# Kernel tuning notes

Hardware: AMD Instinct MI355X
Metric: run time of the kernel (lower is better)

The kernel has to match this reference:

```python
import jax, jax.numpy as jnp
import numpy as np

DROPOUT_P = 0.1  # original source passed p=1 (degenerate, zeros output); 0.1 used for a meaningful baseline


def setup_inputs() -> dict:
    key0 = jax.random.key(0)
    ks = jax.random.split(key0, 11)
    B, H, L, D, DQK, DV = 2, 8, 2048, 1024, 64, 64
    return {
        "query": jax.random.normal(ks[0], (B, H, L, D), jnp.float32),
        "key":   jax.random.normal(ks[1], (B, H, L, D), jnp.float32),
        "value": jax.random.normal(ks[2], (B, H, L, D), jnp.float32),
        "Wq": jax.random.normal(ks[3], (D, DQK), jnp.float32) * (D ** -0.5),
        "bq": jax.random.normal(ks[4], (DQK,), jnp.float32) * 0.02,
        "Wk": jax.random.normal(ks[5], (D, DQK), jnp.float32) * (D ** -0.5),
        "bk": jax.random.normal(ks[6], (DQK,), jnp.float32) * 0.02,
        "Wv": jax.random.normal(ks[7], (D, DV), jnp.float32) * (D ** -0.5),
        "bv": jax.random.normal(ks[8], (DV,), jnp.float32) * 0.02,
        "Wo": jax.random.normal(ks[9], (DV, D), jnp.float32) * (DV ** -0.5),
        "bo": jax.random.normal(ks[10], (D,), jnp.float32) * 0.02,
    }


def reference(query, key, value, Wq, bq, Wk, bk, Wv, bv, Wo, bo):
    # Per-head linear projections on 4D inputs (B,H,L,d_model)
    q = query @ Wq + bq            # (B,H,Lq,dqk)
    k = key @ Wk + bk              # (B,H,Lk,dqk)
    v = value @ Wv + bv            # (B,H,Lk,dv)
    # Quirky scale from source: q.size(2)*q.size(3)/key.size(2) * key.size(-1)**-0.5
    dk = (q.shape[2] * q.shape[3] / key.shape[2]) * (key.shape[-1] ** -0.5)
    scores = jnp.einsum('bhqd,bhkd->bhqk', q, k) * jnp.float32(dk)
    attn = jax.nn.softmax(scores, axis=-1)
    # Deterministic dropout with fixed key (inverted-scale, matching F.dropout)
    keep = jax.random.bernoulli(jax.random.key(42), 1.0 - DROPOUT_P, attn.shape)
    attn = jnp.where(keep, attn / (1.0 - DROPOUT_P), jnp.float32(0.0))
    out = jnp.einsum('bhqk,bhkd->bhqd', attn, v)  # (B,H,Lq,dv)
    return out @ Wo + bo                           # (B,H,Lq,d_model)
```

## Files before the change

### kernel.cpp

```cpp
#include <hip/hip_runtime.h>
#include <stdint.h>

typedef _Float16 f16;
typedef __attribute__((ext_vector_type(8))) _Float16 f16x8;
typedef __attribute__((ext_vector_type(4))) float f32x4;

__device__ __forceinline__ uint32_t rotl1(uint32_t x, uint32_t n){
  return __builtin_amdgcn_alignbit(x, x, 32u - n);
}
__device__ __forceinline__ uint32_t tf_bits(uint32_t i){
  const uint32_t ks1 = 42u, ks2 = 0x1BD11BDAu ^ 42u;
  uint32_t x0 = 0u, x1 = i + 42u;
#define R4(a,b,c,d) \
  x0 += x1; x1 = rotl1(x1,a); x1 ^= x0; \
  x0 += x1; x1 = rotl1(x1,b); x1 ^= x0; \
  x0 += x1; x1 = rotl1(x1,c); x1 ^= x0; \
  x0 += x1; x1 = rotl1(x1,d); x1 ^= x0;
  R4(13,15,26,6)  x0 += ks1; x1 += ks2 + 1u;
  R4(17,29,16,24) x0 += ks2; x1 += 2u;
  R4(13,15,26,6)               x1 += ks1 + 3u;
  R4(17,29,16,24) x0 += ks1; x1 += ks2 + 4u;
  R4(13,15,26,6)  x0 += ks2; x1 += 5u;
#undef R4
  return x0 ^ x1;
}

template<int PACKED>
__global__ __launch_bounds__(256) void proj_kernel(
    const float* __restrict__ query, const float* __restrict__ keyp, const float* __restrict__ value,
    const float* __restrict__ Wq, const float* __restrict__ bq,
    const float* __restrict__ Wk, const float* __restrict__ bk,
    const float* __restrict__ Wv, const float* __restrict__ bv,
    const float* __restrict__ Wo,
    f16* __restrict__ qp, f16* __restrict__ kp, f16* __restrict__ vpT,
    f16* __restrict__ WoT)
{
  __shared__ __align__(16) f16 Alds[64][40];
  __shared__ __align__(16) f16 Wlds[64][40];
  const int bid = blockIdx.x;
  const int tid = threadIdx.x;
  const int lane = tid & 63, wave = tid >> 6;
  const int llo = lane & 15, lhi = lane >> 4;

  int p;
  if (PACKED == 0){
    if (bid < 256){
      int t = bid*256 + tid;
      int n = t & 1023, k = t >> 10;
      WoT[(long)n*64 + k] = (f16)Wo[(long)k*1024 + n];
      return;
    }
    p = bid - 256;
  } else {
    p = 768 + bid;
  }

  const int which = p >> 9;
  const long m0 = (long)(p & 511) * 64;
  const float* A    = which==0 ? query : (which==1 ? keyp : value);
  const float* W    = which==0 ? Wq    : (which==1 ? Wk   : Wv);
  const float* bias = which==0 ? bq    : (which==1 ? bk   : bv);

  f32x4 acc[4];
  #pragma unroll
  for (int n=0;n<4;n++){
    float bb = bias[16*n + llo];
    acc[n][0]=bb; acc[n][1]=bb; acc[n][2]=bb; acc[n][3]=bb;
  }

  const int ar = tid >> 2;
  const int ac = (tid & 3) * 8;
  const int wcol = tid & 63;
  const int wk = (tid >> 6) * 8;

  for (int k0 = 0; k0 < 1024; k0 += 32){
    {
      const float* asrc = A + (m0 + ar)*1024 + k0 + ac;
      float4 v0 = *(const float4*)asrc;
      float4 v1 = *(const float4*)(asrc + 4);
      if (PACKED == 0){
        f16* ad = &Alds[ar][ac];
        ad[0]=(f16)v0.x; ad[1]=(f16)v0.y; ad[2]=(f16)v0.z; ad[3]=(f16)v0.w;
        ad[4]=(f16)v1.x; ad[5]=(f16)v1.y; ad[6]=(f16)v1.z; ad[7]=(f16)v1.w;
      } else {
        union { f16 h[8]; f16x8 v; } aw;
        aw.h[0]=(f16)v0.x; aw.h[1]=(f16)v0.y; aw.h[2]=(f16)v0.z; aw.h[3]=(f16)v0.w;
        aw.h[4]=(f16)v1.x; aw.h[5]=(f16)v1.y; aw.h[6]=(f16)v1.z; aw.h[7]=(f16)v1.w;
        *(f16x8*)&Alds[ar][ac] = aw.v;
      }
      f16 wt[8];
      #pragma unroll
      for (int j=0;j<8;j++) wt[j] = (f16)W[(long)(k0+wk+j)*64 + wcol];
      *(f16x8*)&Wlds[wcol][wk] = *(f16x8*)wt;
    }
    __syncthreads();
    f16x8 af = *(const f16x8*)&Alds[wave*16 + llo][lhi*8];
    #pragma unroll
    for (int n=0;n<4;n++){
      f16x8 bf = *(const f16x8*)&Wlds[16*n + llo][lhi*8];
      acc[n] = __builtin_amdgcn_mfma_f32_16x16x32_f16(af, bf, acc[n], 0,0,0);
    }
    __syncthreads();
  }

  if (which < 2){
    const float scale = (which==0) ? 2.0f : 1.0f;
    f16* dst = (which==0) ? qp : kp;
    #pragma unroll
    for (int n=0;n<4;n++)
      #pragma unroll
      for (int j=0;j<4;j++){
        long row = m0 + wave*16 + lhi*4 + j;
        dst[row*64 + 16*n + llo] = (f16)(acc[n][j]*scale);
      }
  } else {
    long row0 = m0 + wave*16 + lhi*4;
    long bh = row0 >> 11;
    long lr = row0 & 2047;
    #pragma unroll
    for (int n=0;n<4;n++){
      union { f16 h[4]; ushort4 u; } pk;
      #pragma unroll
      for (int j=0;j<4;j++) pk.h[j] = (f16)acc[n][j];
      *(ushort4*)&vpT[(bh*64 + 16*n + llo)*2048 + lr] = pk.u;
    }
  }
}

__global__ __launch_bounds__(256) void flash_kernel(
    const f16* __restrict__ qp, const f16* __restrict__ kp, const f16* __restrict__ vpT,
    float* __restrict__ Opart, float* __restrict__ Mp, float* __restrict__ Lp)
{
  __shared__ __align__(16) f16 Klds[64][72];
  __shared__ __align__(16) f16 Vlds[64][72];
  __shared__ __align__(16) f16 Plds[4][16][72];
  __shared__ unsigned short Idl[4][1024];
  const int tid = threadIdx.x;
  const int lane = tid & 63, wave = tid >> 6;
  const int llo = lane & 15, lhi = lane >> 4;
  const int bh = blockIdx.y;
  const int q0 = blockIdx.x * 64;
  const int kvh = blockIdx.z;

  const f16* qbase = qp + ((long)bh*2048 + q0 + wave*16 + llo)*64 + lhi*8;
  f16x8 qf0 = *(const f16x8*)qbase;
  f16x8 qf1 = *(const f16x8*)(qbase + 32);

  f32x4 O[4];
  float mrun[4], lrun[4];
  #pragma unroll
  for (int n=0;n<4;n++){ O[n][0]=0.f;O[n][1]=0.f;O[n][2]=0.f;O[n][3]=0.f; }
  #pragma unroll
  for (int j=0;j<4;j++){ mrun[j] = -__builtin_inff(); lrun[j]=0.f; }

  const int sr = tid >> 2;
  const int sc = (tid & 3) * 16;
  const f16* kbh = kp + (long)bh*2048*64;
  const f16* vbh = vpT + (long)bh*64*2048;
  uint32_t base_w = (uint32_t)((bh*2048 + q0 + wave*16)*2048) + (uint32_t)(kvh*1024);

  const int kvlo = kvh*1024, kvhi = kvlo + 1024;
  for (int kv0 = kvlo; kv0 < kvhi; kv0 += 64, base_w += 64u){
    {
      const f16* src = kbh + (long)(kv0 + sr)*64 + sc;
      f16x8 t0 = *(const f16x8*)src;
      f16x8 t1 = *(const f16x8*)(src+8);
      *(f16x8*)&Klds[sr][sc]   = t0;
      *(f16x8*)&Klds[sr][sc+8] = t1;
      const f16* vsrc = vbh + (long)sr*2048 + kv0 + sc;
      f16x8 u0 = *(const f16x8*)vsrc;
      f16x8 u1 = *(const f16x8*)(vsrc+8);
      *(f16x8*)&Vlds[sr][sc]   = u0;
      *(f16x8*)&Vlds[sr][sc+8] = u1;
    }
    __syncthreads();

    f32x4 s[4];
    #pragma unroll
    for (int n=0;n<4;n++){ s[n][0]=0.f;s[n][1]=0.f;s[n][2]=0.f;s[n][3]=0.f; }
    #pragma unroll
    for (int n=0;n<4;n++){
      f16x8 kf0 = *(const f16x8*)&Klds[16*n+llo][lhi*8];
      s[n] = __builtin_amdgcn_mfma_f32_16x16x32_f16(qf0, kf0, s[n], 0,0,0);
      f16x8 kf1 = *(const f16x8*)&Klds[16*n+llo][32+lhi*8];
      s[n] = __builtin_amdgcn_mfma_f32_16x16x32_f16(qf1, kf1, s[n], 0,0,0);
    }
    float pmax[4];
    #pragma unroll
    for (int j=0;j<4;j++)
      pmax[j] = fmaxf(fmaxf(s[0][j],s[1][j]), fmaxf(s[2][j],s[3][j]));
    #pragma unroll
    for (int off=1; off<16; off<<=1){
      #pragma unroll
      for (int j=0;j<4;j++) pmax[j] = fmaxf(pmax[j], __shfl_xor(pmax[j], off));
    }
    float esc[4];
    #pragma unroll
    for (int j=0;j<4;j++){
      float mnew = fmaxf(mrun[j], pmax[j]);
      esc[j] = __expf(mrun[j] - mnew);
      mrun[j] = mnew;
    }
    float p[4][4]; float lsum[4] = {0.f,0.f,0.f,0.f};
    #pragma unroll
    for (int n=0;n<4;n++)
      #pragma unroll
      for (int j=0;j<4;j++){
        p[n][j] = __expf(s[n][j] - mrun[j]);
        lsum[j] += p[n][j];
      }
    #pragma unroll
    for (int off=1; off<16; off<<=1){
      #pragma unroll
      for (int j=0;j<4;j++) lsum[j] += __shfl_xor(lsum[j], off);
    }
    #pragma unroll
    for (int j=0;j<4;j++) lrun[j] = lrun[j]*esc[j] + lsum[j];
    #pragma unroll
    for (int n=0;n<4;n++)
      #pragma unroll
      for (int j=0;j<4;j++) O[n][j] *= esc[j];

    uint32_t cnt = 0;
    #pragma unroll
    for (int j=0;j<4;j++){
      #pragma unroll
      for (int n=0;n<4;n++){
        float pm = p[n][j]*(1.0f/0.9f);
        bool surv = pm > 0x1.0p-25f;
        Plds[wave][lhi*4+j][16*n+llo] = (f16)pm;
        unsigned long long mk = __ballot(surv);
        if (mk){
          uint32_t pre = __builtin_amdgcn_mbcnt_hi((uint32_t)(mk>>32),
                         __builtin_amdgcn_mbcnt_lo((uint32_t)mk, 0u));
          if (surv)
            Idl[wave][cnt + pre] = (unsigned short)((j<<8)|(n<<6)|lane);
          cnt += (uint32_t)__builtin_popcountll(mk);
        }
      }
    }
    for (uint32_t pb = 0; pb < cnt; pb += 64){
      uint32_t idx = pb + (uint32_t)lane;
      if (idx < cnt){
        uint32_t id = (uint32_t)Idl[wave][idx];
        uint32_t jj = (id>>8)&3u, nn = (id>>6)&3u, ln = id & 63u;
        uint32_t i = base_w + (ln>>4)*8192u + jj*2048u + nn*16u + (ln&15u);
        uint32_t bits = tf_bits(i);
        if (bits >= 0xE6666600u)
          Plds[wave][(ln>>4)*4+jj][16*nn+(ln&15u)] = (f16)0;
      }
    }

    f16x8 pa0 = *(const f16x8*)&Plds[wave][llo][lhi*8];
    f16x8 pa1 = *(const f16x8*)&Plds[wave][llo][32+lhi*8];
    #pragma unroll
    for (int n=0;n<4;n++){
      f16x8 vf0 = *(const f16x8*)&Vlds[16*n+llo][lhi*8];
      O[n] = __builtin_amdgcn_mfma_f32_16x16x32_f16(pa0, vf0, O[n], 0,0,0);
      f16x8 vf1 = *(const f16x8*)&Vlds[16*n+llo][32+lhi*8];
      O[n] = __builtin_amdgcn_mfma_f32_16x16x32_f16(pa1, vf1, O[n], 0,0,0);
    }
    __syncthreads();
  }

  const long pr = ((long)kvh*16 + bh)*2048 + q0 + wave*16 + lhi*4;
  #pragma unroll
  for (int n=0;n<4;n++)
    #pragma unroll
    for (int j=0;j<4;j++)
      Opart[(pr + j)*64 + 16*n + llo] = O[n][j];
  if (llo == 0){
    const long mr = (long)kvh*32768 + bh*2048 + q0 + wave*16 + lhi*4;
    #pragma unroll
    for (int j=0;j<4;j++){ Mp[mr + j] = mrun[j]; Lp[mr + j] = lrun[j]; }
  }
}

__global__ __launch_bounds__(256) void combine_kernel(
    const float* __restrict__ Opart, const float* __restrict__ Mp, const float* __restrict__ Lp,
    const f16* __restrict__ WoT, const float* __restrict__ bo, float* __restrict__ out)
{
  const int tid = threadIdx.x;
  const int lane = tid & 63, wave = tid >> 6;
  const int llo = lane & 15, lhi = lane >> 4;
  const long m0 = (long)blockIdx.x * 64;
  const int nb = blockIdx.y * 256;

  const long gr = m0 + wave*16 + llo;
  float m0v = Mp[gr], m1v = Mp[32768 + gr];
  float l0  = Lp[gr], l1  = Lp[32768 + gr];
  float M  = fmaxf(m0v, m1v);
  float e0 = __expf(m0v - M), e1 = __expf(m1v - M);
  float rl = 1.0f / (l0*e0 + l1*e1);
  float w0 = e0*rl, w1 = e1*rl;

  const float* o0 = Opart + gr*64;
  const float* o1 = Opart + 2097152 + gr*64;
  f16x8 af0, af1;
  {
    union { f16 h[8]; f16x8 v; } u;
    const int c0 = lhi*8;
    #pragma unroll
    for (int e=0;e<8;e++) u.h[e] = (f16)(o0[c0+e]*w0 + o1[c0+e]*w1);
    af0 = u.v;
    const int c1 = 32 + lhi*8;
    #pragma unroll
    for (int e=0;e<8;e++) u.h[e] = (f16)(o0[c1+e]*w0 + o1[c1+e]*w1);
    af1 = u.v;
  }

  const long robase = m0 + wave*16 + lhi*4;
  for (int n0 = nb; n0 < nb+256; n0 += 16){
    f16x8 b0 = *(const f16x8*)&WoT[(long)(n0+llo)*64 + lhi*8];
    f16x8 b1 = *(const f16x8*)&WoT[(long)(n0+llo)*64 + 32 + lhi*8];
    float bb = bo[n0+llo];
    f32x4 c; c[0]=bb; c[1]=bb; c[2]=bb; c[3]=bb;
    c = __builtin_amdgcn_mfma_f32_16x16x32_f16(af0, b0, c, 0,0,0);
    c = __builtin_amdgcn_mfma_f32_16x16x32_f16(af1, b1, c, 0,0,0);
    #pragma unroll
    for (int j=0;j<4;j++)
      out[(robase + j)*1024 + n0 + llo] = c[j];
  }
}

extern "C" void kernel_launch(void* const* d_in, const int* in_sizes, int n_in,
                              void* d_out, int out_size, void* d_ws, size_t ws_size,
                              hipStream_t stream){
  const float* query = (const float*)d_in[0];
  const float* key   = (const float*)d_in[1];
  const float* value = (const float*)d_in[2];
  const float* Wq = (const float*)d_in[3];
  const float* bq = (const float*)d_in[4];
  const float* Wk = (const float*)d_in[5];
  const float* bk = (const float*)d_in[6];
  const float* Wv = (const float*)d_in[7];
  const float* bv = (const float*)d_in[8];
  const float* Wo = (const float*)d_in[9];
  const float* bo = (const float*)d_in[10];
  float* out = (float*)d_out;

  char* ws = (char*)d_ws;
  f16* qp      = (f16*)(ws);
  f16* kp      = (f16*)(ws + ((size_t)4<<20));
  f16* vpT     = (f16*)(ws + ((size_t)8<<20));
  float* Opart = (float*)(ws + ((size_t)12<<20));
  float* Mp    = (float*)(ws + ((size_t)28<<20));
  float* Lp    = (float*)(ws + ((size_t)28<<20) + (256<<10));
  f16* WoT     = (f16*)(ws + ((size_t)28<<20) + (512<<10));

  proj_kernel<0><<<dim3(1024), dim3(256), 0, stream>>>(
      query,key,value,Wq,bq,Wk,bk,Wv,bv,Wo,qp,kp,vpT,WoT);
  proj_kernel<1><<<dim3(768), dim3(256), 0, stream>>>(
      query,key,value,Wq,bq,Wk,bk,Wv,bv,Wo,qp,kp,vpT,WoT);
  flash_kernel<<<dim3(32,16,2), dim3(256), 0, stream>>>(qp,kp,vpT,Opart,Mp,Lp);
  combine_kernel<<<dim3(512,4), dim3(256), 0, stream>>>(Opart,Mp,Lp,WoT,bo,out);
}
```

Measured before the change: 257.9 us.

## Generalize KV split to four partitions and stage output stores through LDS

```diff
diff --git a/kernel.cpp b/kernel.cpp
--- a/kernel.cpp
+++ b/kernel.cpp
@@ -141,6 +141,8 @@
   const int bh = blockIdx.y;
   const int q0 = blockIdx.x * 64;
   const int kvh = blockIdx.z;
+  const int kvt = 2048 / gridDim.z;
+  const int kvlo = kvh * kvt, kvhi = kvlo + kvt;
 
   const f16* qbase = qp + ((long)bh*2048 + q0 + wave*16 + llo)*64 + lhi*8;
   f16x8 qf0 = *(const f16x8*)qbase;
@@ -157,9 +159,8 @@
   const int sc = (tid & 3) * 16;
   const f16* kbh = kp + (long)bh*2048*64;
   const f16* vbh = vpT + (long)bh*64*2048;
-  uint32_t base_w = (uint32_t)((bh*2048 + q0 + wave*16)*2048) + (uint32_t)(kvh*1024);
-
-  const int kvlo = kvh*1024, kvhi = kvlo + 1024;
+  uint32_t base_w = (uint32_t)((bh*2048 + q0 + wave*16)*2048) + (uint32_t)kvlo;
+
   for (int kv0 = kvlo; kv0 < kvhi; kv0 += 64, base_w += 64u){
     {
       const f16* src = kbh + (long)(kv0 + sr)*64 + sc;
@@ -263,14 +264,15 @@
     __syncthreads();
   }
 
-  const long pr = ((long)kvh*16 + bh)*2048 + q0 + wave*16 + lhi*4;
+  const long rbase = (long)bh*2048 + q0 + wave*16 + lhi*4;
+  const long pr = ((long)kvh*32768 + rbase)*64;
   #pragma unroll
   for (int n=0;n<4;n++)
     #pragma unroll
     for (int j=0;j<4;j++)
-      Opart[(pr + j)*64 + 16*n + llo] = O[n][j];
+      Opart[pr + (long)j*64 + 16*n + llo] = O[n][j];
   if (llo == 0){
-    const long mr = (long)kvh*32768 + bh*2048 + q0 + wave*16 + lhi*4;
+    const long mr = (long)kvh*32768 + rbase;
     #pragma unroll
     for (int j=0;j<4;j++){ Mp[mr + j] = mrun[j]; Lp[mr + j] = lrun[j]; }
   }
@@ -278,8 +280,10 @@
 
 __global__ __launch_bounds__(256) void combine_kernel(
     const float* __restrict__ Opart, const float* __restrict__ Mp, const float* __restrict__ Lp,
-    const f16* __restrict__ WoT, const float* __restrict__ bo, float* __restrict__ out)
+    const f16* __restrict__ WoT, const float* __restrict__ bo, float* __restrict__ out,
+    int ns)
 {
+  __shared__ __align__(16) float Ot[64][68];
   const int tid = threadIdx.x;
   const int lane = tid & 63, wave = tid >> 6;
   const int llo = lane & 15, lhi = lane >> 4;
@@ -287,39 +291,67 @@
   const int nb = blockIdx.y * 256;
 
   const long gr = m0 + wave*16 + llo;
-  float m0v = Mp[gr], m1v = Mp[32768 + gr];
-  float l0  = Lp[gr], l1  = Lp[32768 + gr];
-  float M  = fmaxf(m0v, m1v);
-  float e0 = __expf(m0v - M), e1 = __expf(m1v - M);
-  float rl = 1.0f / (l0*e0 + l1*e1);
-  float w0 = e0*rl, w1 = e1*rl;
-
-  const float* o0 = Opart + gr*64;
-  const float* o1 = Opart + 2097152 + gr*64;
+  float mv[4], lv[4], w[4];
+  float M = -__builtin_inff();
+  for (int s=0;s<ns;s++){
+    mv[s] = Mp[(long)s*32768 + gr];
+    lv[s] = Lp[(long)s*32768 + gr];
+    M = fmaxf(M, mv[s]);
+  }
+  float denom = 0.f;
+  for (int s=0;s<ns;s++){ w[s] = __expf(mv[s] - M); denom += lv[s]*w[s]; }
+  float rl = 1.0f / denom;
+  for (int s=0;s<ns;s++) w[s] *= rl;
+
+  float a0[8] = {0,0,0,0,0,0,0,0}, a1[8] = {0,0,0,0,0,0,0,0};
+  for (int s=0;s<ns;s++){
+    const float* os = Opart + ((long)s*32768 + gr)*64;
+    float4 x0 = *(const float4*)(os + lhi*8);
+    float4 x1 = *(const float4*)(os + lhi*8 + 4);
+    float4 y0 = *(const float4*)(os + 32 + lhi*8);
+    float4 y1 = *(const float4*)(os + 32 + lhi*8 + 4);
+    a0[0]+=x0.x*w[s]; a0[1]+=x0.y*w[s]; a0[2]+=x0.z*w[s]; a0[3]+=x0.w*w[s];
+    a0[4]+=x1.x*w[s]; a0[5]+=x1.y*w[s]; a0[6]+=x1.z*w[s]; a0[7]+=x1.w*w[s];
+    a1[0]+=y0.x*w[s]; a1[1]+=y0.y*w[s]; a1[2]+=y0.z*w[s]; a1[3]+=y0.w*w[s];
+    a1[4]+=y1.x*w[s]; a1[5]+=y1.y*w[s]; a1[6]+=y1.z*w[s]; a1[7]+=y1.w*w[s];
+  }
   f16x8 af0, af1;
   {
     union { f16 h[8]; f16x8 v; } u;
-    const int c0 = lhi*8;
-    #pragma unroll
-    for (int e=0;e<8;e++) u.h[e] = (f16)(o0[c0+e]*w0 + o1[c0+e]*w1);
+    #pragma unroll
+    for (int e=0;e<8;e++) u.h[e] = (f16)a0[e];
     af0 = u.v;
-    const int c1 = 32 + lhi*8;
-    #pragma unroll
-    for (int e=0;e<8;e++) u.h[e] = (f16)(o0[c1+e]*w0 + o1[c1+e]*w1);
+    #pragma unroll
+    for (int e=0;e<8;e++) u.h[e] = (f16)a1[e];
     af1 = u.v;
   }
 
-  const long robase = m0 + wave*16 + lhi*4;
-  for (int n0 = nb; n0 < nb+256; n0 += 16){
-    f16x8 b0 = *(const f16x8*)&WoT[(long)(n0+llo)*64 + lhi*8];
-    f16x8 b1 = *(const f16x8*)&WoT[(long)(n0+llo)*64 + 32 + lhi*8];
-    float bb = bo[n0+llo];
-    f32x4 c; c[0]=bb; c[1]=bb; c[2]=bb; c[3]=bb;
-    c = __builtin_amdgcn_mfma_f32_16x16x32_f16(af0, b0, c, 0,0,0);
-    c = __builtin_amdgcn_mfma_f32_16x16x32_f16(af1, b1, c, 0,0,0);
-    #pragma unroll
-    for (int j=0;j<4;j++)
-      out[(robase + j)*1024 + n0 + llo] = c[j];
+  const int wr = tid >> 2;
+  const int wc = (tid & 3) * 16;
+  for (int g = 0; g < 4; ++g){
+    #pragma unroll
+    for (int sub = 0; sub < 4; ++sub){
+      const int n0 = nb + g*64 + sub*16;
+      f16x8 b0 = *(const f16x8*)&WoT[(long)(n0+llo)*64 + lhi*8];
+      f16x8 b1 = *(const f16x8*)&WoT[(long)(n0+llo)*64 + 32 + lhi*8];
+      float bb = bo[n0+llo];
+      f32x4 c; c[0]=bb; c[1]=bb; c[2]=bb; c[3]=bb;
+      c = __builtin_amdgcn_mfma_f32_16x16x32_f16(af0, b0, c, 0,0,0);
+      c = __builtin_amdgcn_mfma_f32_16x16x32_f16(af1, b1, c, 0,0,0);
+      #pragma unroll
+      for (int j=0;j<4;j++)
+        Ot[wave*16 + lhi*4 + j][sub*16 + llo] = c[j];
+    }
+    __syncthreads();
+    {
+      float* dst = out + (m0 + wr)*1024 + nb + g*64 + wc;
+      const float* srcr = &Ot[wr][wc];
+      *(float4*)(dst)      = *(const float4*)(srcr);
+      *(float4*)(dst + 4)  = *(const float4*)(srcr + 4);
+      *(float4*)(dst + 8)  = *(const float4*)(srcr + 8);
+      *(float4*)(dst + 12) = *(const float4*)(srcr + 12);
+    }
+    __syncthreads();
   }
 }
 
@@ -339,19 +371,23 @@
   const float* bo = (const float*)d_in[10];
   float* out = (float*)d_out;
 
+  const size_t need4 = ((size_t)12<<20) + ((size_t)32<<20) + (2<<20);
+  const int ns = (ws_size >= need4) ? 4 : 2;
+
   char* ws = (char*)d_ws;
   f16* qp      = (f16*)(ws);
   f16* kp      = (f16*)(ws + ((size_t)4<<20));
   f16* vpT     = (f16*)(ws + ((size_t)8<<20));
   float* Opart = (float*)(ws + ((size_t)12<<20));
-  float* Mp    = (float*)(ws + ((size_t)28<<20));
-  float* Lp    = (float*)(ws + ((size_t)28<<20) + (256<<10));
-  f16* WoT     = (f16*)(ws + ((size_t)28<<20) + (512<<10));
+  char*  tail  = ws + ((size_t)12<<20) + ((size_t)ns<<23);
+  float* Mp    = (float*)(tail);
+  float* Lp    = (float*)(tail + ((size_t)ns<<17));
+  f16* WoT     = (f16*)(tail + ((size_t)ns<<18));
 
   proj_kernel<0><<<dim3(1024), dim3(256), 0, stream>>>(
       query,key,value,Wq,bq,Wk,bk,Wv,bv,Wo,qp,kp,vpT,WoT);
   proj_kernel<1><<<dim3(768), dim3(256), 0, stream>>>(
       query,key,value,Wq,bq,Wk,bk,Wv,bv,Wo,qp,kp,vpT,WoT);
-  flash_kernel<<<dim3(32,16,2), dim3(256), 0, stream>>>(qp,kp,vpT,Opart,Mp,Lp);
-  combine_kernel<<<dim3(512,4), dim3(256), 0, stream>>>(Opart,Mp,Lp,WoT,bo,out);
-}
+  flash_kernel<<<dim3(32,16,ns), dim3(256), 0, stream>>>(qp,kp,vpT,Opart,Mp,Lp);
+  combine_kernel<<<dim3(512,4), dim3(256), 0, stream>>>(Opart,Mp,Lp,WoT,bo,out,ns);
+}
```

Result: slower. 287.1 us (+11.3%).

## Skip redundant softmax rescale, defer row-sum reduction, stage combine output through LDS

Applied to the files above, without the earlier changes.

```diff
diff --git a/kernel.cpp b/kernel.cpp
--- a/kernel.cpp
+++ b/kernel.cpp
@@ -141,25 +141,25 @@
   const int bh = blockIdx.y;
   const int q0 = blockIdx.x * 64;
   const int kvh = blockIdx.z;
+  const int kvlo = kvh * 1024, kvhi = kvlo + 1024;
 
   const f16* qbase = qp + ((long)bh*2048 + q0 + wave*16 + llo)*64 + lhi*8;
   f16x8 qf0 = *(const f16x8*)qbase;
   f16x8 qf1 = *(const f16x8*)(qbase + 32);
 
   f32x4 O[4];
-  float mrun[4], lrun[4];
+  float mrun[4], lp[4];
   #pragma unroll
   for (int n=0;n<4;n++){ O[n][0]=0.f;O[n][1]=0.f;O[n][2]=0.f;O[n][3]=0.f; }
   #pragma unroll
-  for (int j=0;j<4;j++){ mrun[j] = -__builtin_inff(); lrun[j]=0.f; }
+  for (int j=0;j<4;j++){ mrun[j] = -__builtin_inff(); lp[j]=0.f; }
 
   const int sr = tid >> 2;
   const int sc = (tid & 3) * 16;
   const f16* kbh = kp + (long)bh*2048*64;
   const f16* vbh = vpT + (long)bh*64*2048;
-  uint32_t base_w = (uint32_t)((bh*2048 + q0 + wave*16)*2048) + (uint32_t)(kvh*1024);
-
-  const int kvlo = kvh*1024, kvhi = kvlo + 1024;
+  uint32_t base_w = (uint32_t)((bh*2048 + q0 + wave*16)*2048) + (uint32_t)kvlo;
+
   for (int kv0 = kvlo; kv0 < kvhi; kv0 += 64, base_w += 64u){
     {
       const f16* src = kbh + (long)(kv0 + sr)*64 + sc;
@@ -194,32 +194,30 @@
       #pragma unroll
       for (int j=0;j<4;j++) pmax[j] = fmaxf(pmax[j], __shfl_xor(pmax[j], off));
     }
-    float esc[4];
-    #pragma unroll
-    for (int j=0;j<4;j++){
-      float mnew = fmaxf(mrun[j], pmax[j]);
-      esc[j] = __expf(mrun[j] - mnew);
-      mrun[j] = mnew;
-    }
-    float p[4][4]; float lsum[4] = {0.f,0.f,0.f,0.f};
+    bool up = (pmax[0]>mrun[0]) | (pmax[1]>mrun[1]) |
+              (pmax[2]>mrun[2]) | (pmax[3]>mrun[3]);
+    if (__any(up)){
+      float esc[4];
+      #pragma unroll
+      for (int j=0;j<4;j++){
+        float mnew = fmaxf(mrun[j], pmax[j]);
+        esc[j] = __expf(mrun[j] - mnew);
+        mrun[j] = mnew;
+      }
+      #pragma unroll
+      for (int j=0;j<4;j++) lp[j] *= esc[j];
+      #pragma unroll
+      for (int n=0;n<4;n++)
+        #pragma unroll
+        for (int j=0;j<4;j++) O[n][j] *= esc[j];
+    }
+    float p[4][4];
     #pragma unroll
     for (int n=0;n<4;n++)
       #pragma unroll
-      for (int j=0;j<4;j++){
-        p[n][j] = __expf(s[n][j] - mrun[j]);
-        lsum[j] += p[n][j];
-      }
-    #pragma unroll
-    for (int off=1; off<16; off<<=1){
-      #pragma unroll
-      for (int j=0;j<4;j++) lsum[j] += __shfl_xor(lsum[j], off);
-    }
-    #pragma unroll
-    for (int j=0;j<4;j++) lrun[j] = lrun[j]*esc[j] + lsum[j];
-    #pragma unroll
-    for (int n=0;n<4;n++)
-      #pragma unroll
-      for (int j=0;j<4;j++) O[n][j] *= esc[j];
+      for (int j=0;j<4;j++) p[n][j] = __expf(s[n][j] - mrun[j]);
+    #pragma unroll
+    for (int j=0;j<4;j++) lp[j] += p[0][j] + p[1][j] + p[2][j] + p[3][j];
 
     uint32_t cnt = 0;
     #pragma unroll
@@ -263,14 +261,24 @@
     __syncthreads();
   }
 
-  const long pr = ((long)kvh*16 + bh)*2048 + q0 + wave*16 + lhi*4;
+  float lrun[4];
+  #pragma unroll
+  for (int j=0;j<4;j++) lrun[j] = lp[j];
+  #pragma unroll
+  for (int off=1; off<16; off<<=1){
+    #pragma unroll
+    for (int j=0;j<4;j++) lrun[j] += __shfl_xor(lrun[j], off);
+  }
+
+  const long rbase = (long)bh*2048 + q0 + wave*16 + lhi*4;
+  const long pr = ((long)kvh*32768 + rbase)*64;
   #pragma unroll
   for (int n=0;n<4;n++)
     #pragma unroll
     for (int j=0;j<4;j++)
-      Opart[(pr + j)*64 + 16*n + llo] = O[n][j];
+      Opart[pr + (long)j*64 + 16*n + llo] = O[n][j];
   if (llo == 0){
-    const long mr = (long)kvh*32768 + bh*2048 + q0 + wave*16 + lhi*4;
+    const long mr = (long)kvh*32768 + rbase;
     #pragma unroll
     for (int j=0;j<4;j++){ Mp[mr + j] = mrun[j]; Lp[mr + j] = lrun[j]; }
   }
@@ -280,11 +288,12 @@
     const float* __restrict__ Opart, const float* __restrict__ Mp, const float* __restrict__ Lp,
     const f16* __restrict__ WoT, const float* __restrict__ bo, float* __restrict__ out)
 {
+  __shared__ __align__(16) float Ot[64][68];
   const int tid = threadIdx.x;
   const int lane = tid & 63, wave = tid >> 6;
   const int llo = lane & 15, lhi = lane >> 4;
   const long m0 = (long)blockIdx.x * 64;
-  const int nb = blockIdx.y * 256;
+  const int nb = blockIdx.y * 512;
 
   const long gr = m0 + wave*16 + llo;
   float m0v = Mp[gr], m1v = Mp[32768 + gr];
@@ -298,28 +307,53 @@
   const float* o1 = Opart + 2097152 + gr*64;
   f16x8 af0, af1;
   {
+    float4 x0 = *(const float4*)(o0 + lhi*8);
+    float4 x1 = *(const float4*)(o0 + lhi*8 + 4);
+    float4 y0 = *(const float4*)(o1 + lhi*8);
+    float4 y1 = *(const float4*)(o1 + lhi*8 + 4);
     union { f16 h[8]; f16x8 v; } u;
-    const int c0 = lhi*8;
-    #pragma unroll
-    for (int e=0;e<8;e++) u.h[e] = (f16)(o0[c0+e]*w0 + o1[c0+e]*w1);
+    u.h[0]=(f16)(x0.x*w0+y0.x*w1); u.h[1]=(f16)(x0.y*w0+y0.y*w1);
+    u.h[2]=(f16)(x0.z*w0+y0.z*w1); u.h[3]=(f16)(x0.w*w0+y0.w*w1);
+    u.h[4]=(f16)(x1.x*w0+y1.x*w1); u.h[5]=(f16)(x1.y*w0+y1.y*w1);
+    u.h[6]=(f16)(x1.z*w0+y1.z*w1); u.h[7]=(f16)(x1.w*w0+y1.w*w1);
     af0 = u.v;
-    const int c1 = 32 + lhi*8;
-    #pragma unroll
-    for (int e=0;e<8;e++) u.h[e] = (f16)(o0[c1+e]*w0 + o1[c1+e]*w1);
+    x0 = *(const float4*)(o0 + 32 + lhi*8);
+    x1 = *(const float4*)(o0 + 32 + lhi*8 + 4);
+    y0 = *(const float4*)(o1 + 32 + lhi*8);
+    y1 = *(const float4*)(o1 + 32 + lhi*8 + 4);
+    u.h[0]=(f16)(x0.x*w0+y0.x*w1); u.h[1]=(f16)(x0.y*w0+y0.y*w1);
+    u.h[2]=(f16)(x0.z*w0+y0.z*w1); u.h[3]=(f16)(x0.w*w0+y0.w*w1);
+    u.h[4]=(f16)(x1.x*w0+y1.x*w1); u.h[5]=(f16)(x1.y*w0+y1.y*w1);
+    u.h[6]=(f16)(x1.z*w0+y1.z*w1); u.h[7]=(f16)(x1.w*w0+y1.w*w1);
     af1 = u.v;
   }
 
-  const long robase = m0 + wave*16 + lhi*4;
-  for (int n0 = nb; n0 < nb+256; n0 += 16){
-    f16x8 b0 = *(const f16x8*)&WoT[(long)(n0+llo)*64 + lhi*8];
-    f16x8 b1 = *(const f16x8*)&WoT[(long)(n0+llo)*64 + 32 + lhi*8];
-    float bb = bo[n0+llo];
-    f32x4 c; c[0]=bb; c[1]=bb; c[2]=bb; c[3]=bb;
-    c = __builtin_amdgcn_mfma_f32_16x16x32_f16(af0, b0, c, 0,0,0);
-    c = __builtin_amdgcn_mfma_f32_16x16x32_f16(af1, b1, c, 0,0,0);
-    #pragma unroll
-    for (int j=0;j<4;j++)
-      out[(robase + j)*1024 + n0 + llo] = c[j];
+  const int wr = tid >> 2;
+  const int wc = (tid & 3) * 16;
+  for (int g = 0; g < 8; ++g){
+    #pragma unroll
+    for (int sub = 0; sub < 4; ++sub){
+      const int n0 = nb + g*64 + sub*16;
+      f16x8 b0 = *(const f16x8*)&WoT[(long)(n0+llo)*64 + lhi*8];
+      f16x8 b1 = *(const f16x8*)&WoT[(long)(n0+llo)*64 + 32 + lhi*8];
+      float bb = bo[n0+llo];
+      f32x4 c; c[0]=bb; c[1]=bb; c[2]=bb; c[3]=bb;
+      c = __builtin_amdgcn_mfma_f32_16x16x32_f16(af0, b0, c, 0,0,0);
+      c = __builtin_amdgcn_mfma_f32_16x16x32_f16(af1, b1, c, 0,0,0);
+      #pragma unroll
+      for (int j=0;j<4;j++)
+        Ot[wave*16 + lhi*4 + j][sub*16 + llo] = c[j];
+    }
+    __syncthreads();
+    {
+      float* dst = out + (m0 + wr)*1024 + nb + g*64 + wc;
+      const float* srcr = &Ot[wr][wc];
+      *(float4*)(dst)      = *(const float4*)(srcr);
+      *(float4*)(dst + 4)  = *(const float4*)(srcr + 4);
+      *(float4*)(dst + 8)  = *(const float4*)(srcr + 8);
+      *(float4*)(dst + 12) = *(const float4*)(srcr + 12);
+    }
+    __syncthreads();
   }
 }
 
@@ -353,5 +387,5 @@
   proj_kernel<1><<<dim3(768), dim3(256), 0, stream>>>(
       query,key,value,Wq,bq,Wk,bk,Wv,bv,Wo,qp,kp,vpT,WoT);
   flash_kernel<<<dim3(32,16,2), dim3(256), 0, stream>>>(qp,kp,vpT,Opart,Mp,Lp);
-  combine_kernel<<<dim3(512,4), dim3(256), 0, stream>>>(Opart,Mp,Lp,WoT,bo,out);
-}
+  combine_kernel<<<dim3(512,2), dim3(256), 0, stream>>>(Opart,Mp,Lp,WoT,bo,out);
+}
```

Result: slower. 283.1 us (+9.8%).
